# Optimization experiments

Measured on AMD Instinct MI355X. Metric: run time of the kernel, lower is better.

The kernel has to match this reference:

```python
import jax, jax.numpy as jnp
import numpy as np

B, S, HID = 4, 2048, 2048
NH, NKV, D = 16, 8, 128
RK, RV = 16, 16
HPG = NH // NKV
SCALING = D ** -0.5
NEG = -1e9


def _rope(x, cos, sin):
    # x: [B, S, H, D]; cos/sin: [S, D//2]. Gemma split-half complex rotation.
    x1, x2 = jnp.split(x, 2, axis=-1)
    c = cos[None, :, None, :]
    s = sin[None, :, None, :]
    return jnp.concatenate([x1 * c - x2 * s, x1 * s + x2 * c], axis=-1)


def setup_inputs() -> dict:
    key = jax.random.key(0)
    ks = jax.random.split(key, 8)
    hidden_states = jax.random.normal(ks[0], (B, S, HID), dtype=jnp.float32)
    # RoPE frequencies (theta=10000)
    inv_freq = 1.0 / (10000.0 ** (np.arange(0, D, 2, dtype=np.float32) / D))
    ang = np.arange(S, dtype=np.float32)[:, None] * inv_freq[None, :]
    freqs_cos = jnp.asarray(np.cos(ang), dtype=jnp.float32)
    freqs_sin = jnp.asarray(np.sin(ang), dtype=jnp.float32)
    kv_write_indices = jnp.arange(S, dtype=jnp.int32)
    # causal additive mask [1,1,S,S]
    causal = jnp.tril(jnp.ones((S, S), dtype=bool))
    mask = jnp.where(causal, 0.0, NEG).astype(jnp.float32)[None, None]
    sc = 0.02
    W_q = jax.random.normal(ks[1], (NH * D, HID), dtype=jnp.float32) * sc
    W_k = jax.random.normal(ks[2], (NKV * D, HID), dtype=jnp.float32) * sc
    W_v = jax.random.normal(ks[3], (NKV * D, HID), dtype=jnp.float32) * sc
    o_proj_w = jax.random.normal(ks[4], (HID, NH * D), dtype=jnp.float32) * sc
    V_r_basis = jax.random.normal(ks[5], (NH, D, RK), dtype=jnp.float32) * (D ** -0.5)
    Z_v_basis = jax.random.normal(ks[6], (NKV, D, RV), dtype=jnp.float32) * (D ** -0.5)
    return {"hidden_states": hidden_states, "freqs_cos": freqs_cos, "freqs_sin": freqs_sin,
            "kv_write_indices": kv_write_indices, "mask": mask, "W_q": W_q, "W_k": W_k,
            "W_v": W_v, "o_proj_w": o_proj_w, "V_r_basis": V_r_basis, "Z_v_basis": Z_v_basis}


def reference(hidden_states, freqs_cos, freqs_sin, kv_write_indices, mask,
              W_q, W_k, W_v, o_proj_w, V_r_basis, Z_v_basis):
    bsz, q_len, _ = hidden_states.shape
    q = (hidden_states @ W_q.T).reshape(bsz, q_len, NH, D)
    k = (hidden_states @ W_k.T).reshape(bsz, q_len, NKV, D)
    v = (hidden_states @ W_v.T).reshape(bsz, q_len, NKV, D)

    # project K per-head onto its group's basis (vectorized over the head loop)
    head_to_group = jnp.arange(NH) // HPG                       # [NH]
    k_per_head = k[:, :, head_to_group, :]                      # [B,S,NH,D]
    pk = jnp.einsum('bshd,hdr->bshr', k_per_head, V_r_basis)    # [B,S,NH,RK]
    pv = jnp.einsum('bqgd,gdr->bqgr', v, Z_v_basis)             # [B,S,NKV,RV]

    # factorized cache write (scatter along seq dim), prefill: kv_seq_len = S
    kv_seq_len = q_len
    cache_pk = jnp.zeros((bsz, kv_seq_len, NH, RK), hidden_states.dtype)
    cache_pv = jnp.zeros((bsz, kv_seq_len, NKV, RV), hidden_states.dtype)
    cache_pk = cache_pk.at[:, kv_write_indices].set(pk)
    cache_pv = cache_pv.at[:, kv_write_indices].set(pv)

    # reconstruct K/V from compressed cache
    k_hat = jnp.einsum('bshr,hrd->bshd', cache_pk, jnp.swapaxes(V_r_basis, -1, -2))
    v_hat = jnp.einsum('bsgr,grd->bsgd', cache_pv, jnp.swapaxes(Z_v_basis, -1, -2))

    # RoPE post-reconstruction
    q_rot = _rope(q, freqs_cos[:q_len], freqs_sin[:q_len])
    k_rot = _rope(k_hat, freqs_cos[:kv_seq_len], freqs_sin[:kv_seq_len])

    # GQA: repeat kv heads
    v_g = jnp.repeat(v_hat, HPG, axis=2)                        # [B,S,NH,D]

    scores = jnp.einsum('bqhd,bkhd->bhqk', q_rot, k_rot) * SCALING
    scores = scores + mask[:, :, :q_len, :kv_seq_len]
    probs = jax.nn.softmax(scores.astype(jnp.float32), axis=-1).astype(hidden_states.dtype)
    out = jnp.einsum('bhqk,bkhd->bqhd', probs, v_g)
    out = out.reshape(bsz, q_len, NH * D)
    return out @ o_proj_w.T
```

## Files before the change

kernel.cpp:

```cpp
#include <hip/hip_runtime.h>

typedef unsigned short ushort8 __attribute__((ext_vector_type(8)));
typedef short s16x8 __attribute__((ext_vector_type(8)));
typedef float f32x4 __attribute__((ext_vector_type(4)));

#define AS1 __attribute__((address_space(1)))
#define AS3 __attribute__((address_space(3)))

#define B_    4
#define S_    2048
#define HID_  2048
#define NH_   16
#define NKV_  8
#define D_    128
#define RK_   16
#define SCALING_ 0.08838834764831845f
#define NEGBIG   -1.0e30f

__device__ __forceinline__ float bf2f(unsigned short u) {
  union { unsigned int i; float f; } x; x.i = ((unsigned int)u) << 16; return x.f;
}
__device__ __forceinline__ unsigned short f2bf(float f) {
  union { float f; unsigned int i; } x; x.f = f;
  unsigned int r = x.i + 0x7fffu + ((x.i >> 16) & 1u);
  return (unsigned short)(r >> 16);
}

__global__ __launch_bounds__(256) void cvt_bf16(const float* __restrict__ in,
                                                unsigned short* __restrict__ out,
                                                int n8) {
  int i = blockIdx.x * 256 + threadIdx.x;
  const int stride = gridDim.x * 256;
  for (; i < n8; i += stride) {
    const float4 a = ((const float4*)in)[i * 2];
    const float4 b = ((const float4*)in)[i * 2 + 1];
    ushort8 u;
    u[0] = f2bf(a.x); u[1] = f2bf(a.y); u[2] = f2bf(a.z); u[3] = f2bf(a.w);
    u[4] = f2bf(b.x); u[5] = f2bf(b.y); u[6] = f2bf(b.z); u[7] = f2bf(b.w);
    *(ushort8*)&out[i * 8] = u;
  }
}

template<bool CBF>
__global__ __launch_bounds__(256) void gemm_mfma(const unsigned short* __restrict__ A,
                                                 const unsigned short* __restrict__ Bb,
                                                 void* __restrict__ C_,
                                                 int M, int N, int K) {
  __shared__ unsigned short Ash[128 * 64];
  __shared__ unsigned short Bsh[128 * 64];
  const int tid = threadIdx.x;
  const int w = tid >> 6, l = tid & 63, lg = l >> 4, ll = l & 15;
  const int wr = w >> 1, wc = w & 1;
  const int flat = blockIdx.y * gridDim.x + blockIdx.x;
  const int cpx = (gridDim.x * gridDim.y) >> 3;
  const int swz = (flat & 7) * cpx + (flat >> 3);
  const int bm = (swz / gridDim.x) * 128, bn = (swz % gridDim.x) * 128;

  f32x4 acc[4][4];
#pragma unroll
  for (int i = 0; i < 4; i++)
#pragma unroll
    for (int j = 0; j < 4; j++) acc[i][j] = (f32x4){0.f, 0.f, 0.f, 0.f};

  const int srow = tid >> 3;
  const int sslot = tid & 7;

  for (int k0 = 0; k0 < K; k0 += 64) {
    __syncthreads();
#pragma unroll
    for (int c = 0; c < 4; ++c) {
      const int row = c * 32 + srow;
      const int ss = sslot ^ (row & 7);
      const unsigned short* srcA = &A[(size_t)(bm + row) * K + k0 + ss * 8];
      const unsigned short* srcB = &Bb[(size_t)(bn + row) * K + k0 + ss * 8];
      char* dstA = ((char*)Ash) + c * 4096 + w * 1024;
      char* dstB = ((char*)Bsh) + c * 4096 + w * 1024;
      __builtin_amdgcn_global_load_lds((const AS1 void*)srcA, (AS3 void*)dstA, 16, 0, 0);
      __builtin_amdgcn_global_load_lds((const AS1 void*)srcB, (AS3 void*)dstB, 16, 0, 0);
    }
    __syncthreads();

#pragma unroll
    for (int ks = 0; ks < 2; ++ks) {
      s16x8 af[4], bf_[4];
#pragma unroll
      for (int mi = 0; mi < 4; ++mi) {
        const int row = wr * 64 + mi * 16 + ll;
        af[mi] = *(const s16x8*)&Ash[row * 64 + (((ks * 4 + lg) ^ (row & 7)) * 8)];
      }
#pragma unroll
      for (int ni = 0; ni < 4; ++ni) {
        const int row = wc * 64 + ni * 16 + ll;
        bf_[ni] = *(const s16x8*)&Bsh[row * 64 + (((ks * 4 + lg) ^ (row & 7)) * 8)];
      }
#pragma unroll
      for (int mi = 0; mi < 4; ++mi)
#pragma unroll
        for (int ni = 0; ni < 4; ++ni)
          acc[mi][ni] = __builtin_amdgcn_mfma_f32_16x16x32_bf16(af[mi], bf_[ni], acc[mi][ni], 0, 0, 0);
    }
  }

#pragma unroll
  for (int mi = 0; mi < 4; ++mi)
#pragma unroll
    for (int ni = 0; ni < 4; ++ni)
#pragma unroll
      for (int j = 0; j < 4; ++j) {
        const int row = bm + wr * 64 + mi * 16 + lg * 4 + j;
        const int col = bn + wc * 64 + ni * 16 + ll;
        if (CBF) ((unsigned short*)C_)[(size_t)row * N + col] = f2bf(acc[mi][ni][j]);
        else     ((float*)C_)[(size_t)row * N + col] = acc[mi][ni][j];
      }
}

__global__ __launch_bounds__(256) void rope_q(unsigned short* __restrict__ q,
                                              const float* __restrict__ cosT,
                                              const float* __restrict__ sinT) {
  const int p = blockIdx.x * 256 + threadIdx.x;
  const int d = p & 63;
  const int h = (p >> 6) & 15;
  const int s = (p >> 10) & 2047;
  const int b = p >> 21;
  const size_t base = (((size_t)b * S_ + s) * NH_ + h) * D_ + d;
  const float x1 = bf2f(q[base]), x2 = bf2f(q[base + 64]);
  const float c = cosT[s * 64 + d], sn = sinT[s * 64 + d];
  q[base]      = f2bf((x1 * c - x2 * sn) * SCALING_);
  q[base + 64] = f2bf((x1 * sn + x2 * c) * SCALING_);
}

__global__ __launch_bounds__(256) void pkpv_make(const unsigned short* __restrict__ k_raw,
                                                 const unsigned short* __restrict__ v_raw,
                                                 const float* __restrict__ Vr,
                                                 const float* __restrict__ Zv,
                                                 float* __restrict__ pk,
                                                 float* __restrict__ pv) {
  const int s = blockIdx.x, b = blockIdx.y;
  const int tid = threadIdx.x;
  __shared__ float kb[NKV_ * D_];
  __shared__ float vb[NKV_ * D_];
  {
    const size_t o = ((size_t)b * S_ + s) * (NKV_ * D_) + tid * 4;
    ushort4 ku = *(const ushort4*)&k_raw[o];
    kb[tid * 4 + 0] = bf2f(ku.x); kb[tid * 4 + 1] = bf2f(ku.y);
    kb[tid * 4 + 2] = bf2f(ku.z); kb[tid * 4 + 3] = bf2f(ku.w);
    ushort4 vu = *(const ushort4*)&v_raw[o];
    vb[tid * 4 + 0] = bf2f(vu.x); vb[tid * 4 + 1] = bf2f(vu.y);
    vb[tid * 4 + 2] = bf2f(vu.z); vb[tid * 4 + 3] = bf2f(vu.w);
  }
  __syncthreads();
  {
    const int h = tid >> 4, r = tid & 15, g = h >> 1;
    float a = 0.f;
    const float* vr = &Vr[(size_t)h * D_ * RK_ + r];
    const float* kk = &kb[g * D_];
#pragma unroll 8
    for (int d = 0; d < D_; d++) a += kk[d] * vr[d * RK_];
    pk[(((size_t)b * S_ + s) * NH_ + h) * RK_ + r] = a;
  }
  if (tid < 128) {
    const int g = tid >> 4, r = tid & 15;
    float a = 0.f;
    const float* zv = &Zv[(size_t)g * D_ * RK_ + r];
    const float* vv = &vb[g * D_];
#pragma unroll 8
    for (int d = 0; d < D_; d++) a += vv[d] * zv[d * RK_];
    pv[(((size_t)b * S_ + s) * NKV_ + g) * RK_ + r] = a;
  }
}

__global__ __launch_bounds__(256) void expand_k(const float* __restrict__ pk,
                                                const float* __restrict__ Vr,
                                                const float* __restrict__ cosT,
                                                const float* __restrict__ sinT,
                                                unsigned short* __restrict__ kr) {
  const int s0 = blockIdx.x * 32, h = blockIdx.y, b = blockIdx.z;
  const int tid = threadIdx.x;
  __shared__ float pkS[32][17];
  if (tid < 128) {
    const int r_ = tid >> 2, c4 = (tid & 3) * 4;
    float4 v = *(const float4*)&pk[(((size_t)b * S_ + s0 + r_) * NH_ + h) * RK_ + c4];
    pkS[r_][c4 + 0] = v.x; pkS[r_][c4 + 1] = v.y;
    pkS[r_][c4 + 2] = v.z; pkS[r_][c4 + 3] = v.w;
  }
  __syncthreads();
  const int row = tid >> 3, dl = tid & 7;
  float kh[16];
#pragma unroll
  for (int j = 0; j < 16; j++) {
    const int d = dl + 8 * j;
    const float4* w = (const float4*)&Vr[((size_t)h * D_ + d) * RK_];
    float a = 0.f;
#pragma unroll
    for (int q4 = 0; q4 < 4; q4++) {
      float4 wv = w[q4];
      a += pkS[row][q4 * 4 + 0] * wv.x + pkS[row][q4 * 4 + 1] * wv.y
         + pkS[row][q4 * 4 + 2] * wv.z + pkS[row][q4 * 4 + 3] * wv.w;
    }
    kh[j] = a;
  }
  const int pos = s0 + row;
  const size_t o = (((size_t)b * NH_ + h) * S_ + pos) * D_;
#pragma unroll
  for (int j = 0; j < 8; j++) {
    const int d = dl + 8 * j;
    const float c = cosT[pos * 64 + d], sn = sinT[pos * 64 + d];
    kr[o + d]      = f2bf(kh[j] * c - kh[j + 8] * sn);
    kr[o + d + 64] = f2bf(kh[j] * sn + kh[j + 8] * c);
  }
}

__global__ __launch_bounds__(256) void expand_v(const float* __restrict__ pv,
                                                const float* __restrict__ Zv,
                                                unsigned short* __restrict__ vh) {
  const int s0 = blockIdx.x * 32, g = blockIdx.y, b = blockIdx.z;
  const int tid = threadIdx.x;
  __shared__ float pvS[32][17];
  if (tid < 128) {
    const int r_ = tid >> 2, c4 = (tid & 3) * 4;
    float4 v = *(const float4*)&pv[(((size_t)b * S_ + s0 + r_) * NKV_ + g) * RK_ + c4];
    pvS[r_][c4 + 0] = v.x; pvS[r_][c4 + 1] = v.y;
    pvS[r_][c4 + 2] = v.z; pvS[r_][c4 + 3] = v.w;
  }
  __syncthreads();
  const int row = tid >> 3, dl = tid & 7;
  const size_t o = (((size_t)b * NKV_ + g) * S_ + s0 + row) * D_;
#pragma unroll
  for (int j = 0; j < 16; j++) {
    const int d = dl + 8 * j;
    const float4* w = (const float4*)&Zv[((size_t)g * D_ + d) * RK_];
    float a = 0.f;
#pragma unroll
    for (int q4 = 0; q4 < 4; q4++) {
      float4 wv = w[q4];
      a += pvS[row][q4 * 4 + 0] * wv.x + pvS[row][q4 * 4 + 1] * wv.y
         + pvS[row][q4 * 4 + 2] * wv.z + pvS[row][q4 * 4 + 3] * wv.w;
    }
    vh[o + d] = f2bf(a);
  }
}

__global__ __launch_bounds__(256) void attn_mfma(const unsigned short* __restrict__ q,
                                                 const unsigned short* __restrict__ kr,
                                                 const unsigned short* __restrict__ vh,
                                                 unsigned short* __restrict__ out) {
  const int flat = ((int)blockIdx.z * 16 + (int)blockIdx.y) * 16 + (int)blockIdx.x;
  const int swz = (flat & 7) * 128 + (flat >> 3);
  const int qt = 15 - (swz & 15);
  const int h = (swz >> 4) & 15;
  const int b = swz >> 8;
  const int g = h >> 1;
  const int tid = threadIdx.x;
  const int w = tid >> 6, l = tid & 63, lg = l >> 4, ll = l & 15;

  __shared__ unsigned short Klds[2][64 * 128];
  __shared__ unsigned short Vt[2][128 * 64];
  __shared__ unsigned short Ps[4][32 * 64];

  const int qr0 = qt * 128 + w * 32;
  const int ktmax = 2 * qt + 1;
  const int kmy = 2 * qt + (w >> 1);

  s16x8 qf[2][4];
#pragma unroll
  for (int mi = 0; mi < 2; ++mi)
#pragma unroll
    for (int ks = 0; ks < 4; ++ks)
      qf[mi][ks] = *(const s16x8*)&q[(((size_t)b * S_ + qr0 + mi * 16 + ll) * NH_ + h) * D_ + ks * 32 + lg * 8];

  f32x4 o[2][8];
#pragma unroll
  for (int mi = 0; mi < 2; ++mi)
#pragma unroll
    for (int nd = 0; nd < 8; ++nd) o[mi][nd] = (f32x4){0.f, 0.f, 0.f, 0.f};
  float m_[2][4], l_[2][4];
#pragma unroll
  for (int mi = 0; mi < 2; ++mi)
#pragma unroll
    for (int j = 0; j < 4; ++j) { m_[mi][j] = NEGBIG; l_[mi][j] = 0.f; }

  const unsigned short* kbase = &kr[(((size_t)b * NH_ + h) * S_) * D_];
  const unsigned short* vbase = &vh[(((size_t)b * NKV_ + g) * S_) * D_];
  const int vk = (tid & 31) * 2, d0v = (tid >> 5) * 16;

  ushort8 va0, va1, vb0, vb1;
  {
#pragma unroll
    for (int c = 0; c < 4; ++c) {
      const int ro = c * 16 + w * 4 + lg;
      const int ss = ll ^ (ro & 7);
      const unsigned short* src = kbase + ro * D_ + ss * 8;
      char* dst = ((char*)&Klds[0][0]) + c * 4096 + w * 1024;
      __builtin_amdgcn_global_load_lds((const AS1 void*)src, (AS3 void*)dst, 16, 0, 0);
    }
    const unsigned short* v0 = vbase + (size_t)vk * D_ + d0v;
    va0 = *(const ushort8*)v0; va1 = *(const ushort8*)(v0 + 8);
    vb0 = *(const ushort8*)(v0 + D_); vb1 = *(const ushort8*)(v0 + D_ + 8);
#pragma unroll
    for (int j = 0; j < 8; ++j) {
      const int d1 = d0v + j, d2 = d0v + 8 + j;
      *(unsigned int*)&Vt[0][d1 * 64 + (((vk >> 3) ^ (d1 & 7)) * 8) + (vk & 7)] =
          (unsigned int)va0[j] | ((unsigned int)vb0[j] << 16);
      *(unsigned int*)&Vt[0][d2 * 64 + (((vk >> 3) ^ (d2 & 7)) * 8) + (vk & 7)] =
          (unsigned int)va1[j] | ((unsigned int)vb1[j] << 16);
    }
  }
  __syncthreads();

  for (int kt = 0; kt <= ktmax; ++kt) {
    const int p = kt & 1;
    if (kt < ktmax) {
      const unsigned short* kb2 = kbase + (size_t)(kt + 1) * 64 * D_;
#pragma unroll
      for (int c = 0; c < 4; ++c) {
        const int ro = c * 16 + w * 4 + lg;
        const int ss = ll ^ (ro & 7);
        const unsigned short* src = kb2 + ro * D_ + ss * 8;
        char* dst = ((char*)&Klds[p ^ 1][0]) + c * 4096 + w * 1024;
        __builtin_amdgcn_global_load_lds((const AS1 void*)src, (AS3 void*)dst, 16, 0, 0);
      }
      const unsigned short* v0 = vbase + (size_t)((kt + 1) * 64 + vk) * D_ + d0v;
      va0 = *(const ushort8*)v0; va1 = *(const ushort8*)(v0 + 8);
      vb0 = *(const ushort8*)(v0 + D_); vb1 = *(const ushort8*)(v0 + D_ + 8);
    }

    if (kt <= kmy) {
      f32x4 s[2][4];
#pragma unroll
      for (int mi = 0; mi < 2; ++mi)
#pragma unroll
        for (int ni = 0; ni < 4; ++ni) s[mi][ni] = (f32x4){0.f, 0.f, 0.f, 0.f};
#pragma unroll
      for (int ks = 0; ks < 4; ++ks) {
#pragma unroll
        for (int ni = 0; ni < 4; ++ni) {
          const int row = ni * 16 + ll;
          const s16x8 kf = *(const s16x8*)&Klds[p][row * 128 + (((ks * 4 + lg) ^ (row & 7)) * 8)];
          s[0][ni] = __builtin_amdgcn_mfma_f32_16x16x32_bf16(qf[0][ks], kf, s[0][ni], 0, 0, 0);
          s[1][ni] = __builtin_amdgcn_mfma_f32_16x16x32_bf16(qf[1][ks], kf, s[1][ni], 0, 0, 0);
        }
      }

      const bool diag = (kt == kmy);
      float lm[2][4];
#pragma unroll
      for (int mi = 0; mi < 2; ++mi)
#pragma unroll
        for (int j = 0; j < 4; ++j) {
          if (diag) {
            const int qg = qr0 + mi * 16 + lg * 4 + j;
#pragma unroll
            for (int ni = 0; ni < 4; ++ni)
              if (kt * 64 + ni * 16 + ll > qg) s[mi][ni][j] = NEGBIG;
          }
          lm[mi][j] = fmaxf(fmaxf(s[mi][0][j], s[mi][1][j]),
                            fmaxf(s[mi][2][j], s[mi][3][j]));
        }
      float excess = lm[0][0] - m_[0][0];
#pragma unroll
      for (int mi = 0; mi < 2; ++mi)
#pragma unroll
        for (int j = 0; j < 4; ++j) excess = fmaxf(excess, lm[mi][j] - m_[mi][j]);
      const bool slow = __any(excess > 8.0f);

#pragma unroll
      for (int mi = 0; mi < 2; ++mi)
#pragma unroll
        for (int j = 0; j < 4; ++j) {
          float ps_[4];
          if (slow) {
            float mt = lm[mi][j];
            mt = fmaxf(mt, __shfl_xor(mt, 1));
            mt = fmaxf(mt, __shfl_xor(mt, 2));
            mt = fmaxf(mt, __shfl_xor(mt, 4));
            mt = fmaxf(mt, __shfl_xor(mt, 8));
            const float mnew = fmaxf(m_[mi][j], mt);
            const float al = __expf(m_[mi][j] - mnew);
            m_[mi][j] = mnew;
            float sum = 0.f;
#pragma unroll
            for (int ni = 0; ni < 4; ++ni) { ps_[ni] = __expf(s[mi][ni][j] - mnew); sum += ps_[ni]; }
            l_[mi][j] = l_[mi][j] * al + sum;
#pragma unroll
            for (int nd = 0; nd < 8; ++nd) o[mi][nd][j] *= al;
          } else {
            float sum = 0.f;
#pragma unroll
            for (int ni = 0; ni < 4; ++ni) { ps_[ni] = __expf(s[mi][ni][j] - m_[mi][j]); sum += ps_[ni]; }
            l_[mi][j] += sum;
          }
          const int prow = mi * 16 + lg * 4 + j;
#pragma unroll
          for (int nq = 0; nq < 2; ++nq) {
            unsigned int u;
            asm("v_cvt_pk_bf16_f32 %0, %1, %2" : "=v"(u) : "v"(ps_[nq * 2]), "v"(ps_[nq * 2 + 1]));
            const int c0 = nq * 32 + ll, c1 = nq * 32 + 16 + ll;
            Ps[w][prow * 64 + (((c0 >> 3) ^ (prow & 7)) * 8) + (ll & 7)] = (unsigned short)u;
            Ps[w][prow * 64 + (((c1 >> 3) ^ (prow & 7)) * 8) + (ll & 7)] = (unsigned short)(u >> 16);
          }
        }

      s16x8 pa[2][2];
#pragma unroll
      for (int mi = 0; mi < 2; ++mi)
#pragma unroll
        for (int ks2 = 0; ks2 < 2; ++ks2) {
          const int prow = mi * 16 + ll;
          pa[mi][ks2] = *(const s16x8*)&Ps[w][prow * 64 + (((ks2 * 4 + lg) ^ (prow & 7)) * 8)];
        }
#pragma unroll
      for (int nd = 0; nd < 8; ++nd) {
#pragma unroll
        for (int ks2 = 0; ks2 < 2; ++ks2) {
          const int vr = nd * 16 + ll;
          const s16x8 vbf = *(const s16x8*)&Vt[p][vr * 64 + (((ks2 * 4 + lg) ^ (vr & 7)) * 8)];
          o[0][nd] = __builtin_amdgcn_mfma_f32_16x16x32_bf16(pa[0][ks2], vbf, o[0][nd], 0, 0, 0);
          o[1][nd] = __builtin_amdgcn_mfma_f32_16x16x32_bf16(pa[1][ks2], vbf, o[1][nd], 0, 0, 0);
        }
      }
    }

    if (kt < ktmax) {
#pragma unroll
      for (int j = 0; j < 8; ++j) {
        const int d1 = d0v + j, d2 = d0v + 8 + j;
        *(unsigned int*)&Vt[p ^ 1][d1 * 64 + (((vk >> 3) ^ (d1 & 7)) * 8) + (vk & 7)] =
            (unsigned int)va0[j] | ((unsigned int)vb0[j] << 16);
        *(unsigned int*)&Vt[p ^ 1][d2 * 64 + (((vk >> 3) ^ (d2 & 7)) * 8) + (vk & 7)] =
            (unsigned int)va1[j] | ((unsigned int)vb1[j] << 16);
      }
    }
    __syncthreads();
  }

#pragma unroll
  for (int mi = 0; mi < 2; ++mi)
#pragma unroll
    for (int j = 0; j < 4; ++j) {
      float ls = l_[mi][j];
      ls += __shfl_xor(ls, 1);
      ls += __shfl_xor(ls, 2);
      ls += __shfl_xor(ls, 4);
      ls += __shfl_xor(ls, 8);
      const float inv = 1.f / ls;
      const size_t rowg = (size_t)b * S_ + qr0 + mi * 16 + lg * 4 + j;
      unsigned short* op = &out[rowg * (NH_ * D_) + h * D_ + ll];
#pragma unroll
      for (int nd = 0; nd < 8; ++nd) op[nd * 16] = f2bf(o[mi][nd][j] * inv);
    }
}

extern "C" void kernel_launch(void* const* d_in, const int* in_sizes, int n_in,
                              void* d_out, int out_size, void* d_ws, size_t ws_size,
                              hipStream_t stream) {
  const float* hidden = (const float*)d_in[0];
  const float* cosT   = (const float*)d_in[1];
  const float* sinT   = (const float*)d_in[2];
  const float* W_q    = (const float*)d_in[5];
  const float* W_k    = (const float*)d_in[6];
  const float* W_v    = (const float*)d_in[7];
  const float* W_o    = (const float*)d_in[8];
  const float* Vr     = (const float*)d_in[9];
  const float* Zv     = (const float*)d_in[10];
  float* out = (float*)d_out;

  char* ws = (char*)d_ws;
  unsigned short* hb     = (unsigned short*)(ws + 0);
  unsigned short* attn_b = (unsigned short*)(ws + 0);
  unsigned short* q_b    = (unsigned short*)(ws + 33554432);
  unsigned short* kraw_b = (unsigned short*)(ws + 67108864);
  unsigned short* vraw_b = (unsigned short*)(ws + 83886080);
  unsigned short* kr_b   = (unsigned short*)(ws + 67108864);
  unsigned short* vh_b   = (unsigned short*)(ws + 100663296);
  unsigned short* WR1    = (unsigned short*)(ws + 117440512);
  unsigned short* WR2    = (unsigned short*)(ws + 125829120);
  float*          pk_f   = (float*)(ws + 117440512);
  float*          pv_f   = (float*)(ws + 125829120);

  const int M = B_ * S_;

  cvt_bf16<<<2048, 256, 0, stream>>>(hidden, hb, (B_ * S_ * HID_) / 8);
  cvt_bf16<<<2048, 256, 0, stream>>>(W_q, WR1, (HID_ * HID_) / 8);
  cvt_bf16<<<2048, 256, 0, stream>>>(W_k, WR2, (NKV_ * D_ * HID_) / 8);

  gemm_mfma<true><<<dim3(16, 64), 256, 0, stream>>>(hb, WR1, q_b,    M, NH_ * D_,  HID_);
  gemm_mfma<true><<<dim3( 8, 64), 256, 0, stream>>>(hb, WR2, kraw_b, M, NKV_ * D_, HID_);
  cvt_bf16<<<2048, 256, 0, stream>>>(W_v, WR2, (NKV_ * D_ * HID_) / 8);
  gemm_mfma<true><<<dim3( 8, 64), 256, 0, stream>>>(hb, WR2, vraw_b, M, NKV_ * D_, HID_);

  rope_q<<<(B_ * S_ * NH_ * 64) / 256, 256, 0, stream>>>(q_b, cosT, sinT);

  pkpv_make<<<dim3(S_, B_), 256, 0, stream>>>(kraw_b, vraw_b, Vr, Zv, pk_f, pv_f);

  expand_k<<<dim3(S_ / 32, NH_, B_), 256, 0, stream>>>(pk_f, Vr, cosT, sinT, kr_b);
  expand_v<<<dim3(S_ / 32, NKV_, B_), 256, 0, stream>>>(pv_f, Zv, vh_b);

  cvt_bf16<<<2048, 256, 0, stream>>>(W_o, WR1, (HID_ * HID_) / 8);

  attn_mfma<<<dim3(16, 16, 4), 256, 0, stream>>>(q_b, kr_b, vh_b, attn_b);

  gemm_mfma<false><<<dim3(16, 64), 256, 0, stream>>>(attn_b, WR1, out, M, HID_, HID_);
}
```

Before: 832.8 us.

## Fuse K/V projections into one GEMM, use exp2 softmax, set MFMA priority

Concatenates the converted W_k and W_v into a single weight buffer so K and V come from one wider GEMM writing an interleaved [K|V] row, which pkpv_make now reads. Folds log2(e) into the Q scaling so the attention softmax can use exp2 instead of exp, and raises the lazy-rescale threshold to match the new base. Wraps the two MFMA loops in s_setprio to favour matrix issue over other waves. Workspace aliasing changes: Wkv shares memory with vh_b, which is written only after the KV GEMM has consumed it.

```diff
diff --git a/kernel.cpp b/kernel.cpp
--- a/kernel.cpp
+++ b/kernel.cpp
@@ -15,6 +15,7 @@
 #define D_    128
 #define RK_   16
 #define SCALING_ 0.08838834764831845f
+#define LOG2E_   1.4426950408889634f
 #define NEGBIG   -1.0e30f
 
 __device__ __forceinline__ float bf2f(unsigned short u) {
@@ -125,12 +126,12 @@
   const size_t base = (((size_t)b * S_ + s) * NH_ + h) * D_ + d;
   const float x1 = bf2f(q[base]), x2 = bf2f(q[base + 64]);
   const float c = cosT[s * 64 + d], sn = sinT[s * 64 + d];
-  q[base]      = f2bf((x1 * c - x2 * sn) * SCALING_);
-  q[base + 64] = f2bf((x1 * sn + x2 * c) * SCALING_);
-}
-
-__global__ __launch_bounds__(256) void pkpv_make(const unsigned short* __restrict__ k_raw,
-                                                 const unsigned short* __restrict__ v_raw,
+  const float sc = SCALING_ * LOG2E_;
+  q[base]      = f2bf((x1 * c - x2 * sn) * sc);
+  q[base + 64] = f2bf((x1 * sn + x2 * c) * sc);
+}
+
+__global__ __launch_bounds__(256) void pkpv_make(const unsigned short* __restrict__ kv_raw,
                                                  const float* __restrict__ Vr,
                                                  const float* __restrict__ Zv,
                                                  float* __restrict__ pk,
@@ -140,11 +141,11 @@
   __shared__ float kb[NKV_ * D_];
   __shared__ float vb[NKV_ * D_];
   {
-    const size_t o = ((size_t)b * S_ + s) * (NKV_ * D_) + tid * 4;
-    ushort4 ku = *(const ushort4*)&k_raw[o];
+    const size_t o = ((size_t)b * S_ + s) * 2048;
+    ushort4 ku = *(const ushort4*)&kv_raw[o + tid * 4];
     kb[tid * 4 + 0] = bf2f(ku.x); kb[tid * 4 + 1] = bf2f(ku.y);
     kb[tid * 4 + 2] = bf2f(ku.z); kb[tid * 4 + 3] = bf2f(ku.w);
-    ushort4 vu = *(const ushort4*)&v_raw[o];
+    ushort4 vu = *(const ushort4*)&kv_raw[o + 1024 + tid * 4];
     vb[tid * 4 + 0] = bf2f(vu.x); vb[tid * 4 + 1] = bf2f(vu.y);
     vb[tid * 4 + 2] = bf2f(vu.z); vb[tid * 4 + 3] = bf2f(vu.w);
   }
@@ -330,6 +331,7 @@
       for (int mi = 0; mi < 2; ++mi)
 #pragma unroll
         for (int ni = 0; ni < 4; ++ni) s[mi][ni] = (f32x4){0.f, 0.f, 0.f, 0.f};
+      __builtin_amdgcn_s_setprio(1);
 #pragma unroll
       for (int ks = 0; ks < 4; ++ks) {
 #pragma unroll
@@ -340,6 +342,7 @@
           s[1][ni] = __builtin_amdgcn_mfma_f32_16x16x32_bf16(qf[1][ks], kf, s[1][ni], 0, 0, 0);
         }
       }
+      __builtin_amdgcn_s_setprio(0);
 
       const bool diag = (kt == kmy);
       float lm[2][4];
@@ -361,7 +364,7 @@
       for (int mi = 0; mi < 2; ++mi)
 #pragma unroll
         for (int j = 0; j < 4; ++j) excess = fmaxf(excess, lm[mi][j] - m_[mi][j]);
-      const bool slow = __any(excess > 8.0f);
+      const bool slow = __any(excess > 11.5f);
 
 #pragma unroll
       for (int mi = 0; mi < 2; ++mi)
@@ -375,18 +378,18 @@
             mt = fmaxf(mt, __shfl_xor(mt, 4));
             mt = fmaxf(mt, __shfl_xor(mt, 8));
             const float mnew = fmaxf(m_[mi][j], mt);
-            const float al = __expf(m_[mi][j] - mnew);
+            const float al = exp2f(m_[mi][j] - mnew);
             m_[mi][j] = mnew;
             float sum = 0.f;
 #pragma unroll
-            for (int ni = 0; ni < 4; ++ni) { ps_[ni] = __expf(s[mi][ni][j] - mnew); sum += ps_[ni]; }
+            for (int ni = 0; ni < 4; ++ni) { ps_[ni] = exp2f(s[mi][ni][j] - mnew); sum += ps_[ni]; }
             l_[mi][j] = l_[mi][j] * al + sum;
 #pragma unroll
             for (int nd = 0; nd < 8; ++nd) o[mi][nd][j] *= al;
           } else {
             float sum = 0.f;
 #pragma unroll
-            for (int ni = 0; ni < 4; ++ni) { ps_[ni] = __expf(s[mi][ni][j] - m_[mi][j]); sum += ps_[ni]; }
+            for (int ni = 0; ni < 4; ++ni) { ps_[ni] = exp2f(s[mi][ni][j] - m_[mi][j]); sum += ps_[ni]; }
             l_[mi][j] += sum;
           }
           const int prow = mi * 16 + lg * 4 + j;
@@ -408,6 +411,7 @@
           const int prow = mi * 16 + ll;
           pa[mi][ks2] = *(const s16x8*)&Ps[w][prow * 64 + (((ks2 * 4 + lg) ^ (prow & 7)) * 8)];
         }
+      __builtin_amdgcn_s_setprio(1);
 #pragma unroll
       for (int nd = 0; nd < 8; ++nd) {
 #pragma unroll
@@ -418,6 +422,7 @@
           o[1][nd] = __builtin_amdgcn_mfma_f32_16x16x32_bf16(pa[1][ks2], vbf, o[1][nd], 0, 0, 0);
         }
       }
+      __builtin_amdgcn_s_setprio(0);
     }
 
     if (kt < ktmax) {
@@ -468,12 +473,11 @@
   unsigned short* hb     = (unsigned short*)(ws + 0);
   unsigned short* attn_b = (unsigned short*)(ws + 0);
   unsigned short* q_b    = (unsigned short*)(ws + 33554432);
-  unsigned short* kraw_b = (unsigned short*)(ws + 67108864);
-  unsigned short* vraw_b = (unsigned short*)(ws + 83886080);
+  unsigned short* kv_b   = (unsigned short*)(ws + 67108864);
   unsigned short* kr_b   = (unsigned short*)(ws + 67108864);
   unsigned short* vh_b   = (unsigned short*)(ws + 100663296);
+  unsigned short* Wkv    = (unsigned short*)(ws + 100663296);
   unsigned short* WR1    = (unsigned short*)(ws + 117440512);
-  unsigned short* WR2    = (unsigned short*)(ws + 125829120);
   float*          pk_f   = (float*)(ws + 117440512);
   float*          pv_f   = (float*)(ws + 125829120);
 
@@ -481,16 +485,15 @@
 
   cvt_bf16<<<2048, 256, 0, stream>>>(hidden, hb, (B_ * S_ * HID_) / 8);
   cvt_bf16<<<2048, 256, 0, stream>>>(W_q, WR1, (HID_ * HID_) / 8);
-  cvt_bf16<<<2048, 256, 0, stream>>>(W_k, WR2, (NKV_ * D_ * HID_) / 8);
-
-  gemm_mfma<true><<<dim3(16, 64), 256, 0, stream>>>(hb, WR1, q_b,    M, NH_ * D_,  HID_);
-  gemm_mfma<true><<<dim3( 8, 64), 256, 0, stream>>>(hb, WR2, kraw_b, M, NKV_ * D_, HID_);
-  cvt_bf16<<<2048, 256, 0, stream>>>(W_v, WR2, (NKV_ * D_ * HID_) / 8);
-  gemm_mfma<true><<<dim3( 8, 64), 256, 0, stream>>>(hb, WR2, vraw_b, M, NKV_ * D_, HID_);
+  cvt_bf16<<<1024, 256, 0, stream>>>(W_k, Wkv, (NKV_ * D_ * HID_) / 8);
+  cvt_bf16<<<1024, 256, 0, stream>>>(W_v, Wkv + (size_t)NKV_ * D_ * HID_, (NKV_ * D_ * HID_) / 8);
+
+  gemm_mfma<true><<<dim3(16, 64), 256, 0, stream>>>(hb, WR1, q_b,  M, 2048, HID_);
+  gemm_mfma<true><<<dim3(16, 64), 256, 0, stream>>>(hb, Wkv, kv_b, M, 2048, HID_);
 
   rope_q<<<(B_ * S_ * NH_ * 64) / 256, 256, 0, stream>>>(q_b, cosT, sinT);
 
-  pkpv_make<<<dim3(S_, B_), 256, 0, stream>>>(kraw_b, vraw_b, Vr, Zv, pk_f, pv_f);
+  pkpv_make<<<dim3(S_, B_), 256, 0, stream>>>(kv_b, Vr, Zv, pk_f, pv_f);
 
   expand_k<<<dim3(S_ / 32, NH_, B_), 256, 0, stream>>>(pk_f, Vr, cosT, sinT, kr_b);
   expand_v<<<dim3(S_ / 32, NKV_, B_), 256, 0, stream>>>(pv_f, Zv, vh_b);
```

Result: slower. 860.1 us (+3.3%).
